# Kernel tuning notes

Hardware: AMD Instinct MI355X
Metric: run time of the kernel (lower is better)

The kernel has to match this reference:

```python
import jax, jax.numpy as jnp
from jax import lax
import numpy as np

DIM = 768
NUM_HEADS = 12
HEAD_DIM = DIM // NUM_HEADS
POOL = 8
LAM1_INIT = 0.5
LAM2_INIT = 0.5
EPS = 1e-6


def rmsnorm(x, w):
    # x / (||x||_2 / sqrt(d) + eps) * w
    d = x.shape[-1]
    rms = jnp.sqrt(jnp.sum(x * x, axis=-1, keepdims=True)) / jnp.sqrt(jnp.asarray(d, x.dtype))
    return x / (rms + EPS) * w


def setup_inputs() -> dict:
    key = jax.random.key(0)
    ks = jax.random.split(key, 10)
    B, H, W = 32, 32, 32
    N = H * W
    x = jax.random.normal(ks[0], (B, N, DIM), dtype=jnp.float32)
    Wqkv = jax.random.normal(ks[1], (3 * DIM, DIM), dtype=jnp.float32) * 0.02
    Wproj = jax.random.normal(ks[2], (DIM, DIM), dtype=jnp.float32) * 0.02
    bproj = jnp.zeros((DIM,), dtype=jnp.float32)
    Wpos = jax.random.normal(ks[3], (HEAD_DIM, HEAD_DIM), dtype=jnp.float32) * 0.02
    Wneg = jax.random.normal(ks[4], (HEAD_DIM, HEAD_DIM), dtype=jnp.float32) * 0.02
    conv_w = jax.random.normal(ks[5], (HEAD_DIM, 1, 3, 3), dtype=jnp.float32) * 0.1  # depthwise OIHW
    lam1 = jnp.asarray(LAM1_INIT, dtype=jnp.float32)
    lam2 = jnp.asarray(LAM2_INIT, dtype=jnp.float32)
    norm1_w = jnp.ones((HEAD_DIM,), dtype=jnp.float32)
    norm2_w = jnp.ones((HEAD_DIM,), dtype=jnp.float32)
    return {"x": x, "Wqkv": Wqkv, "Wproj": Wproj, "bproj": bproj, "Wpos": Wpos,
            "Wneg": Wneg, "conv_w": conv_w, "lam1": lam1, "lam2": lam2,
            "norm1_w": norm1_w, "norm2_w": norm2_w, "H": H, "W": W}


def reference(x, Wqkv, Wproj, bproj, Wpos, Wneg, conv_w, lam1, lam2, norm1_w, norm2_w, H, W):
    B, N, C = x.shape
    h, hd, p = NUM_HEADS, HEAD_DIM, POOL
    scale = hd ** -0.5
    # qkv projection -> [3, B, h, N, hd]
    qkv = (x @ Wqkv.T).reshape(B, N, 3, h, hd).transpose(2, 0, 3, 1, 4)
    q, k, v = qkv[0], qkv[1], qkv[2]
    # depthwise conv + GELU on q in spatial form
    q2 = q.reshape(B, h, H, W, hd).transpose(0, 1, 4, 2, 3).reshape(B * h, hd, H, W)
    qe = lax.conv_general_dilated(q2, conv_w, window_strides=(1, 1), padding='SAME',
                                  feature_group_count=hd,
                                  dimension_numbers=('NCHW', 'OIHW', 'NCHW'))
    qe = jax.nn.gelu(qe, approximate=False)
    # adaptive avg pool to (p, p): exact since H % p == 0
    qp = qe.reshape(B * h, hd, p, H // p, p, W // p).mean(axis=(3, 5))
    t_base = qp.reshape(B, h, hd, p, p).transpose(0, 1, 3, 4, 2).reshape(B, h, p * p, hd)
    # dynamic e+/e- embeddings from global query
    gq = q.mean(axis=2)  # [B, h, hd]
    t_pos = t_base + (gq @ Wpos.T)[:, :, None, :]
    t_neg = t_base + (gq @ Wneg.T)[:, :, None, :]
    # stage 1: pooled contrast tokens attend to k/v
    attn_pos = jax.nn.softmax(jnp.einsum('bhmd,bhnd->bhmn', t_pos, k) * scale, axis=-1)
    v_hat_pos = attn_pos @ v  # [B, h, p*p, hd]
    attn_neg = jax.nn.softmax(jnp.einsum('bhmd,bhnd->bhmn', t_neg, k) * scale, axis=-1)
    v_hat_neg = attn_neg @ v
    v_contrast = rmsnorm(v_hat_pos - lam1 * v_hat_neg, norm1_w) * (1.0 - LAM1_INIT)
    # stage 2: q attends to contrast tokens
    attn1 = jax.nn.softmax(jnp.einsum('bhnd,bhmd->bhnm', q, t_pos) * scale, axis=-1)
    attn2 = jax.nn.softmax(jnp.einsum('bhnd,bhmd->bhnm', q, t_neg) * scale, axis=-1)
    out_patch = (attn1 - lam2 * attn2) @ v_contrast  # [B, h, N, hd]
    out_patch = rmsnorm(out_patch, norm2_w) * (1.0 - LAM2_INIT)
    out_patch = out_patch.transpose(0, 2, 1, 3).reshape(B, N, C)
    out = out_patch @ Wproj.T + bproj
    return out
```

## Files before the change

### kernel.cpp

```cpp
#include <hip/hip_runtime.h>
#include <hip/hip_bf16.h>


typedef __attribute__((ext_vector_type(8))) short short8;
typedef __attribute__((ext_vector_type(4))) short bf16x4;
typedef __attribute__((ext_vector_type(4))) float f32x4;

#define DEV static __device__ __forceinline__

DEV unsigned short f2bf(float f) {
  unsigned int b; __builtin_memcpy(&b, &f, 4);
  unsigned int r = (b + 0x7FFFu + ((b >> 16) & 1u)) >> 16;
  return (unsigned short)r;
}
DEV float bf2f(unsigned short u) {
  unsigned int b = ((unsigned int)u) << 16;
  float f; __builtin_memcpy(&f, &b, 4);
  return f;
}

DEV void gload16(const unsigned short* g, unsigned short* l) {
  __builtin_amdgcn_global_load_lds(
      (const __attribute__((address_space(1))) unsigned int*)g,
      (__attribute__((address_space(3))) unsigned int*)l, 16, 0, 0);
}

constexpr size_t SZ_QKV = (size_t)32 * 12 * 1024 * 64 * 2;
constexpr size_t OFF_Q   = 0;
constexpr size_t OFF_K   = OFF_Q + SZ_QKV;
constexpr size_t OFF_VT  = OFF_K + SZ_QKV;
constexpr size_t OFF_TPB = OFF_VT + SZ_QKV;
constexpr size_t OFF_TNB = OFF_TPB + 3145728;
constexpr size_t OFF_VCT = OFF_TNB + 3145728;
constexpr size_t OFF_OP  = OFF_VCT + 6291456;
constexpr size_t OFF_XB  = OFF_OP + SZ_QKV;
constexpr size_t OFF_WQ  = OFF_XB + SZ_QKV;
constexpr size_t OFF_WP  = OFF_WQ + 3538944;
constexpr size_t OFF_EP  = OFF_WP + 1179648;
constexpr size_t OFF_EN  = OFF_EP + 98304;

__global__ __launch_bounds__(256) void cast_kernel(const float* __restrict__ src,
                                                   unsigned short* __restrict__ dst, int n4) {
  int i = blockIdx.x * 256 + threadIdx.x;
  if (i >= n4) return;
  float4 v = reinterpret_cast<const float4*>(src)[i];
  ushort4 o;
  o.x = f2bf(v.x); o.y = f2bf(v.y); o.z = f2bf(v.z); o.w = f2bf(v.w);
  reinterpret_cast<ushort4*>(dst)[i] = o;
}

__global__ __launch_bounds__(256) void gemm_qkv_kernel(const unsigned short* __restrict__ A,
    const unsigned short* __restrict__ Bm, unsigned short* __restrict__ q,
    unsigned short* __restrict__ k, unsigned short* __restrict__ vt) {
  __shared__ unsigned short As[2 * 128 * 32];
  __shared__ unsigned short Bs[2 * 128 * 32];
  const int t = threadIdx.x;
  const int lane = t & 63;
  const int w = t >> 6;
  const int wm = w >> 1, wn = w & 1;
  const int row0 = blockIdx.y * 128;
  const int col0 = blockIdx.x * 128;
  f32x4 acc[4][4];
#pragma unroll
  for (int i = 0; i < 4; ++i)
#pragma unroll
    for (int j = 0; j < 4; ++j) acc[i][j] = (f32x4){0.f, 0.f, 0.f, 0.f};
  const int l = lane & 15, g = lane >> 4;
  const int srow = lane >> 2, scol = (lane & 3) << 3;
  for (int k0 = 0; k0 < 768; k0 += 64) {
    __syncthreads();
#pragma unroll
    for (int kc = 0; kc < 2; ++kc)
#pragma unroll
      for (int j = 0; j < 2; ++j) {
        const int qs = w * 2 + j;
        const int r = qs * 16 + srow;
        const int cg = k0 + kc * 32 + scol;
        gload16(A + (size_t)(row0 + r) * 768 + cg, As + kc * 4096 + qs * 512);
        gload16(Bm + (size_t)(col0 + r) * 768 + cg, Bs + kc * 4096 + qs * 512);
      }
    __syncthreads();
#pragma unroll
    for (int kc = 0; kc < 2; ++kc) {
      short8 af[4], bfv[4];
#pragma unroll
      for (int mt = 0; mt < 4; ++mt)
        af[mt] = *reinterpret_cast<const short8*>(As + kc * 4096 + (wm * 64 + mt * 16 + l) * 32 + g * 8);
#pragma unroll
      for (int nt = 0; nt < 4; ++nt)
        bfv[nt] = *reinterpret_cast<const short8*>(Bs + kc * 4096 + (wn * 64 + nt * 16 + l) * 32 + g * 8);
#pragma unroll
      for (int mt = 0; mt < 4; ++mt)
#pragma unroll
        for (int nt = 0; nt < 4; ++nt)
          acc[mt][nt] = __builtin_amdgcn_mfma_f32_16x16x32_bf16(af[mt], bfv[nt], acc[mt][nt], 0, 0, 0);
    }
  }
  const int s_ = col0 / 768;
  if (s_ == 2) {
#pragma unroll
    for (int nt = 0; nt < 4; ++nt) {
      const int colin = wn * 64 + nt * 16 + l;
      const int head = ((col0 % 768) + colin) >> 6;
      const int d = colin & 63;
#pragma unroll
      for (int mt = 0; mt < 4; ++mt) {
        const int row = row0 + wm * 64 + mt * 16 + (g << 2);
        const int b = row >> 10, n = row & 1023;
        ushort4 pk;
        pk.x = f2bf(acc[mt][nt][0]); pk.y = f2bf(acc[mt][nt][1]);
        pk.z = f2bf(acc[mt][nt][2]); pk.w = f2bf(acc[mt][nt][3]);
        *reinterpret_cast<ushort4*>(vt + ((((size_t)b * 12 + head) * 64 + d) << 10) + n) = pk;
      }
    }
  } else {
    unsigned short* dst = (s_ == 0) ? q : k;
#pragma unroll
    for (int nt = 0; nt < 4; ++nt) {
      const int colin = wn * 64 + nt * 16 + l;
      const int head = ((col0 % 768) + colin) >> 6;
      const int d = colin & 63;
#pragma unroll
      for (int mt = 0; mt < 4; ++mt) {
#pragma unroll
        for (int r = 0; r < 4; ++r) {
          const int row = row0 + wm * 64 + mt * 16 + (g << 2) + r;
          const int b = row >> 10, n = row & 1023;
          dst[(((size_t)b * 12 + head) * 1024 + n) * 64 + d] = f2bf(acc[mt][nt][r]);
        }
      }
    }
  }
}

__global__ __launch_bounds__(256) void gq_embed_kernel(const unsigned short* __restrict__ qg,
    const float* __restrict__ Wpos, const float* __restrict__ Wneg,
    float* __restrict__ ep, float* __restrict__ en) {
  const int bh = blockIdx.x;
  const unsigned short* qp = qg + (size_t)bh * 65536;
  __shared__ float red2[32][64];
  __shared__ float gq_s[64];
  const int t = threadIdx.x;
  const int c8 = (t & 7) << 3;
  const int part = t >> 3;
  float s[8] = {0.f, 0.f, 0.f, 0.f, 0.f, 0.f, 0.f, 0.f};
  for (int i = 0; i < 32; ++i) {
    const short8 v = *reinterpret_cast<const short8*>(qp + (size_t)(part * 32 + i) * 64 + c8);
#pragma unroll
    for (int j = 0; j < 8; ++j) s[j] += bf2f((unsigned short)v[j]);
  }
#pragma unroll
  for (int j = 0; j < 8; ++j) red2[part][c8 + j] = s[j];
  __syncthreads();
  if (t < 64) {
    float s2 = 0.f;
    for (int p = 0; p < 32; ++p) s2 += red2[p][t];
    gq_s[t] = s2 * (1.0f / 1024.0f);
  }
  __syncthreads();
  if (t < 128) {
    const int d2 = t & 63;
    const float* Wm = (t < 64) ? Wpos : Wneg;
    float e = 0.f;
    for (int dd = 0; dd < 64; ++dd) e += gq_s[dd] * Wm[d2 * 64 + dd];
    (t < 64 ? ep : en)[bh * 64 + d2] = e;
  }
}

__global__ __launch_bounds__(256) void conv_pool_kernel(const unsigned short* __restrict__ qg,
    const float* __restrict__ conv_w, const float* __restrict__ ep,
    const float* __restrict__ en, unsigned short* __restrict__ t_pos,
    unsigned short* __restrict__ t_neg) {
  const int bh = blockIdx.x;
  const int quad = blockIdx.y;
  const unsigned short* qp = qg + (size_t)bh * 65536;
  __shared__ float pool_s[16][64];
  const int t = threadIdx.x;
  const int dg = t & 7, sp = t >> 3;
  const int d0 = dg << 3;
  float cw[3][3][8];
#pragma unroll
  for (int ky = 0; ky < 3; ++ky)
#pragma unroll
    for (int kx = 0; kx < 3; ++kx)
#pragma unroll
      for (int j = 0; j < 8; ++j)
        cw[ky][kx][j] = conv_w[(d0 + j) * 9 + ky * 3 + kx];
#pragma unroll
  for (int pyl = 0; pyl < 2; ++pyl) {
    float win[8] = {0.f, 0.f, 0.f, 0.f, 0.f, 0.f, 0.f, 0.f};
#pragma unroll
    for (int iy = 0; iy < 4; ++iy) {
      const int y = quad * 8 + pyl * 4 + iy;
      float a[8] = {0.f, 0.f, 0.f, 0.f, 0.f, 0.f, 0.f, 0.f};
#pragma unroll
      for (int ky = 0; ky < 3; ++ky) {
        const int yy = y + ky - 1;
        if (yy < 0 || yy > 31) continue;
#pragma unroll
        for (int kx = 0; kx < 3; ++kx) {
          const int xx = sp + kx - 1;
          if (xx < 0 || xx > 31) continue;
          const short8 v = *reinterpret_cast<const short8*>(qp + (size_t)(yy * 32 + xx) * 64 + d0);
#pragma unroll
          for (int j = 0; j < 8; ++j) a[j] += bf2f((unsigned short)v[j]) * cw[ky][kx][j];
        }
      }
#pragma unroll
      for (int j = 0; j < 8; ++j)
        win[j] += 0.5f * a[j] * (1.0f + erff(a[j] * 0.70710678118654752440f));
    }
#pragma unroll
    for (int j = 0; j < 8; ++j) {
      win[j] += __shfl_xor(win[j], 8);
      win[j] += __shfl_xor(win[j], 16);
    }
    if ((sp & 3) == 0) {
      const int px = sp >> 2;
#pragma unroll
      for (int j = 0; j < 8; ++j) pool_s[pyl * 8 + px][d0 + j] = win[j];
    }
  }
  __syncthreads();
#pragma unroll
  for (int i = 0; i < 4; ++i) {
    const int idx = i * 256 + t;
    const int m = idx >> 6, dd = idx & 63;
    const int mg = quad * 16 + m;
    const float base = pool_s[m][dd] * (1.0f / 16.0f);
    t_pos[(size_t)bh * 4096 + mg * 64 + dd] = f2bf(base + ep[bh * 64 + dd]);
    t_neg[(size_t)bh * 4096 + mg * 64 + dd] = f2bf(base + en[bh * 64 + dd]);
  }
}

__global__ __launch_bounds__(256) void stage1_kernel(const unsigned short* __restrict__ kg,
    const unsigned short* __restrict__ vtg, const unsigned short* __restrict__ tpb,
    const unsigned short* __restrict__ tnb, const float* __restrict__ lam1p,
    const float* __restrict__ norm1_w, float* __restrict__ vct) {
  const int bh = blockIdx.x;
  __shared__ unsigned short tp[64 * 72], tn[64 * 72];
  __shared__ unsigned short Ks[64 * 72], Vts[64 * 72];
  const int t = threadIdx.x;
  const int lane = t & 63;
  const int w = t >> 6;
  const int l = lane & 15, g = lane >> 4;
  for (int L = t; L < 512; L += 256) {
    const int r = L >> 3, c = (L & 7) << 3;
    *reinterpret_cast<short8*>(tp + r * 72 + c) =
        *reinterpret_cast<const short8*>(tpb + (size_t)bh * 4096 + r * 64 + c);
    *reinterpret_cast<short8*>(tn + r * 72 + c) =
        *reinterpret_cast<const short8*>(tnb + (size_t)bh * 4096 + r * 64 + c);
  }
  __syncthreads();
  short8 tf[2][2];
#pragma unroll
  for (int h = 0; h < 2; ++h) {
    tf[0][h] = *reinterpret_cast<const short8*>(tp + (w * 16 + l) * 72 + h * 32 + g * 8);
    tf[1][h] = *reinterpret_cast<const short8*>(tn + (w * 16 + l) * 72 + h * 32 + g * 8);
  }
  float Mo[2] = {-1e30f, -1e30f}, Lo[2] = {0.f, 0.f};
  f32x4 acc[2][4];
#pragma unroll
  for (int pp = 0; pp < 2; ++pp)
#pragma unroll
    for (int dt = 0; dt < 4; ++dt) acc[pp][dt] = (f32x4){0.f, 0.f, 0.f, 0.f};
  const size_t kbase = (size_t)bh * 65536;

  for (int n0 = 0; n0 < 1024; n0 += 64) {
    __syncthreads();
    for (int L = t; L < 512; L += 256) {
      const int r = L >> 3, c = (L & 7) << 3;
      *reinterpret_cast<short8*>(Ks + r * 72 + c) =
          *reinterpret_cast<const short8*>(kg + kbase + (size_t)(n0 + r) * 64 + c);
      *reinterpret_cast<short8*>(Vts + r * 72 + c) =
          *reinterpret_cast<const short8*>(vtg + kbase + (size_t)r * 1024 + n0 + c);
    }
    __syncthreads();
    short8 kf[4][2];
#pragma unroll
    for (int tile = 0; tile < 4; ++tile)
#pragma unroll
      for (int h = 0; h < 2; ++h)
        kf[tile][h] = *reinterpret_cast<const short8*>(Ks + (tile * 16 + l) * 72 + h * 32 + g * 8);
    bf16x4 pf[2][4];
#pragma unroll
    for (int pp = 0; pp < 2; ++pp) {
      f32x4 s[4];
#pragma unroll
      for (int tile = 0; tile < 4; ++tile) {
        s[tile] = (f32x4){0.f, 0.f, 0.f, 0.f};
#pragma unroll
        for (int h = 0; h < 2; ++h)
          s[tile] = __builtin_amdgcn_mfma_f32_16x16x32_bf16(kf[tile][h], tf[pp][h], s[tile], 0, 0, 0);
      }
      float p[4][4];
      float tmax = -1e30f;
#pragma unroll
      for (int tile = 0; tile < 4; ++tile)
#pragma unroll
        for (int r = 0; r < 4; ++r) {
          const float v = s[tile][r] * 0.125f;
          p[tile][r] = v;
          tmax = fmaxf(tmax, v);
        }
      tmax = fmaxf(tmax, __shfl_xor(tmax, 16));
      tmax = fmaxf(tmax, __shfl_xor(tmax, 32));
      const float nm = fmaxf(Mo[pp], tmax);
      const float al = __expf(Mo[pp] - nm);
      Mo[pp] = nm;
      float ps = 0.f;
#pragma unroll
      for (int tile = 0; tile < 4; ++tile)
#pragma unroll
        for (int r = 0; r < 4; ++r) {
          const float e = __expf(p[tile][r] - nm);
          p[tile][r] = e;
          ps += e;
        }
      ps += __shfl_xor(ps, 16);
      ps += __shfl_xor(ps, 32);
      Lo[pp] = Lo[pp] * al + ps;
#pragma unroll
      for (int tile = 0; tile < 4; ++tile) {
        bf16x4 pk;
        pk[0] = (short)f2bf(p[tile][0]); pk[1] = (short)f2bf(p[tile][1]);
        pk[2] = (short)f2bf(p[tile][2]); pk[3] = (short)f2bf(p[tile][3]);
        pf[pp][tile] = pk;
      }
      float ar[4];
#pragma unroll
      for (int r = 0; r < 4; ++r) ar[r] = __shfl(al, 4 * g + r);
#pragma unroll
      for (int dt = 0; dt < 4; ++dt)
#pragma unroll
        for (int r = 0; r < 4; ++r) acc[pp][dt][r] *= ar[r];
    }
#pragma unroll
    for (int tile = 0; tile < 4; ++tile)
#pragma unroll
      for (int dt = 0; dt < 4; ++dt) {
        const bf16x4 vf = *reinterpret_cast<const bf16x4*>(Vts + (dt * 16 + l) * 72 + tile * 16 + g * 4);
        acc[0][dt] = __builtin_amdgcn_mfma_f32_16x16x16bf16_1k(pf[0][tile], vf, acc[0][dt], 0, 0, 0);
        acc[1][dt] = __builtin_amdgcn_mfma_f32_16x16x16bf16_1k(pf[1][tile], vf, acc[1][dt], 0, 0, 0);
      }
  }
  const float inv0 = 1.f / Lo[0], inv1 = 1.f / Lo[1];
  float i1r[4], i2r[4];
#pragma unroll
  for (int r = 0; r < 4; ++r) {
    i1r[r] = __shfl(inv0, 4 * g + r);
    i2r[r] = __shfl(inv1, 4 * g + r);
  }
  const float lam1 = lam1p[0];
  float od[4][4], ss[4] = {0.f, 0.f, 0.f, 0.f};
#pragma unroll
  for (int dt = 0; dt < 4; ++dt)
#pragma unroll
    for (int r = 0; r < 4; ++r) {
      const float v = acc[0][dt][r] * i1r[r] - lam1 * (acc[1][dt][r] * i2r[r]);
      od[dt][r] = v;
      ss[r] += v * v;
    }
#pragma unroll
  for (int r = 0; r < 4; ++r) {
    ss[r] += __shfl_xor(ss[r], 1);
    ss[r] += __shfl_xor(ss[r], 2);
    ss[r] += __shfl_xor(ss[r], 4);
    ss[r] += __shfl_xor(ss[r], 8);
  }
  float sc[4];
#pragma unroll
  for (int r = 0; r < 4; ++r) sc[r] = 0.5f / (sqrtf(ss[r]) * 0.125f + 1e-6f);
  const int mb = w * 16 + 4 * g;
#pragma unroll
  for (int dt = 0; dt < 4; ++dt) {
    const int dd = dt * 16 + l;
    const float nw = norm1_w[dd];
#pragma unroll
    for (int r = 0; r < 4; ++r)
      vct[(size_t)bh * 4096 + dd * 64 + mb + r] = od[dt][r] * sc[r] * nw;
  }
}

__global__ __launch_bounds__(256) void stage2_kernel(const unsigned short* __restrict__ qg,
    const unsigned short* __restrict__ tpb, const unsigned short* __restrict__ tnb,
    const float* __restrict__ vct, const float* __restrict__ lam2p,
    const float* __restrict__ norm2_w, unsigned short* __restrict__ opb) {
  const int bh = blockIdx.x;
  const int q0 = blockIdx.y * 64;
  __shared__ unsigned short tp[64 * 72], tn[64 * 72], Qs[64 * 72], Vc[64 * 72];
  const int t = threadIdx.x;
  const int lane = t & 63;
  const int w = t >> 6;
  const int l = lane & 15, g = lane >> 4;
  for (int L = t; L < 512; L += 256) {
    const int r = L >> 3, c = (L & 7) << 3;
    *reinterpret_cast<short8*>(tp + r * 72 + c) =
        *reinterpret_cast<const short8*>(tpb + (size_t)bh * 4096 + r * 64 + c);
    *reinterpret_cast<short8*>(tn + r * 72 + c) =
        *reinterpret_cast<const short8*>(tnb + (size_t)bh * 4096 + r * 64 + c);
    *reinterpret_cast<short8*>(Qs + r * 72 + c) =
        *reinterpret_cast<const short8*>(qg + (size_t)bh * 65536 + (size_t)(q0 + r) * 64 + c);
  }
  for (int L = t; L < 4096; L += 256) {
    const int dd = L >> 6, m = L & 63;
    Vc[dd * 72 + m] = f2bf(vct[(size_t)bh * 4096 + L]);
  }
  __syncthreads();
  short8 qf[2];
#pragma unroll
  for (int h = 0; h < 2; ++h)
    qf[h] = *reinterpret_cast<const short8*>(Qs + (w * 16 + l) * 72 + h * 32 + g * 8);
  bf16x4 vcf[4][4];
#pragma unroll
  for (int tile = 0; tile < 4; ++tile)
#pragma unroll
    for (int dt = 0; dt < 4; ++dt)
      vcf[tile][dt] = *reinterpret_cast<const bf16x4*>(Vc + (dt * 16 + l) * 72 + tile * 16 + g * 4);
  bf16x4 pf[2][4];
#pragma unroll
  for (int pp = 0; pp < 2; ++pp) {
    const unsigned short* tm = pp ? tn : tp;
    f32x4 s[4];
#pragma unroll
    for (int tile = 0; tile < 4; ++tile) {
      s[tile] = (f32x4){0.f, 0.f, 0.f, 0.f};
#pragma unroll
      for (int h = 0; h < 2; ++h) {
        const short8 tfb = *reinterpret_cast<const short8*>(tm + (tile * 16 + l) * 72 + h * 32 + g * 8);
        s[tile] = __builtin_amdgcn_mfma_f32_16x16x32_bf16(tfb, qf[h], s[tile], 0, 0, 0);
      }
    }
    float p[4][4];
    float lmax = -1e30f;
#pragma unroll
    for (int tile = 0; tile < 4; ++tile)
#pragma unroll
      for (int r = 0; r < 4; ++r) {
        const float v = s[tile][r] * 0.125f;
        p[tile][r] = v;
        lmax = fmaxf(lmax, v);
      }
    lmax = fmaxf(lmax, __shfl_xor(lmax, 16));
    lmax = fmaxf(lmax, __shfl_xor(lmax, 32));
    float ps = 0.f;
#pragma unroll
    for (int tile = 0; tile < 4; ++tile)
#pragma unroll
      for (int r = 0; r < 4; ++r) {
        const float e = __expf(p[tile][r] - lmax);
        p[tile][r] = e;
        ps += e;
      }
    ps += __shfl_xor(ps, 16);
    ps += __shfl_xor(ps, 32);
    const float inv = 1.f / ps;
#pragma unroll
    for (int tile = 0; tile < 4; ++tile) {
      bf16x4 pk;
      pk[0] = (short)f2bf(p[tile][0] * inv); pk[1] = (short)f2bf(p[tile][1] * inv);
      pk[2] = (short)f2bf(p[tile][2] * inv); pk[3] = (short)f2bf(p[tile][3] * inv);
      pf[pp][tile] = pk;
    }
  }
  f32x4 a1[4], a2[4];
#pragma unroll
  for (int dt = 0; dt < 4; ++dt) {
    a1[dt] = (f32x4){0.f, 0.f, 0.f, 0.f};
    a2[dt] = (f32x4){0.f, 0.f, 0.f, 0.f};
  }
#pragma unroll
  for (int tile = 0; tile < 4; ++tile)
#pragma unroll
    for (int dt = 0; dt < 4; ++dt) {
      a1[dt] = __builtin_amdgcn_mfma_f32_16x16x16bf16_1k(pf[0][tile], vcf[tile][dt], a1[dt], 0, 0, 0);
      a2[dt] = __builtin_amdgcn_mfma_f32_16x16x16bf16_1k(pf[1][tile], vcf[tile][dt], a2[dt], 0, 0, 0);
    }
  const float lam2 = lam2p[0];
  float od[4][4], ss[4] = {0.f, 0.f, 0.f, 0.f};
#pragma unroll
  for (int dt = 0; dt < 4; ++dt)
#pragma unroll
    for (int r = 0; r < 4; ++r) {
      const float v = a1[dt][r] - lam2 * a2[dt][r];
      od[dt][r] = v;
      ss[r] += v * v;
    }
#pragma unroll
  for (int r = 0; r < 4; ++r) {
    ss[r] += __shfl_xor(ss[r], 1);
    ss[r] += __shfl_xor(ss[r], 2);
    ss[r] += __shfl_xor(ss[r], 4);
    ss[r] += __shfl_xor(ss[r], 8);
  }
  float sc[4];
#pragma unroll
  for (int r = 0; r < 4; ++r) sc[r] = 0.5f / (sqrtf(ss[r]) * 0.125f + 1e-6f);
  const int b = bh / 12, head = bh % 12;
  const size_t ob = ((size_t)b * 1024 + q0 + w * 16 + 4 * g) * 768 + head * 64;
#pragma unroll
  for (int dt = 0; dt < 4; ++dt) {
    const float nw = norm2_w[dt * 16 + l];
#pragma unroll
    for (int r = 0; r < 4; ++r)
      opb[ob + (size_t)r * 768 + dt * 16 + l] = f2bf(od[dt][r] * sc[r] * nw);
  }
}

__global__ __launch_bounds__(256) void gemm_proj_kernel(const unsigned short* __restrict__ A,
    const unsigned short* __restrict__ Bm, const float* __restrict__ bias,
    float* __restrict__ out) {
  __shared__ unsigned short As[2 * 128 * 32];
  __shared__ unsigned short Bs[2 * 128 * 32];
  const int t = threadIdx.x;
  const int lane = t & 63;
  const int w = t >> 6;
  const int wm = w >> 1, wn = w & 1;
  const int row0 = blockIdx.y * 128;
  const int col0 = blockIdx.x * 128;
  f32x4 acc[4][4];
#pragma unroll
  for (int i = 0; i < 4; ++i)
#pragma unroll
    for (int j = 0; j < 4; ++j) acc[i][j] = (f32x4){0.f, 0.f, 0.f, 0.f};
  const int l = lane & 15, g = lane >> 4;
  const int srow = lane >> 2, scol = (lane & 3) << 3;
  for (int k0 = 0; k0 < 768; k0 += 64) {
    __syncthreads();
#pragma unroll
    for (int kc = 0; kc < 2; ++kc)
#pragma unroll
      for (int j = 0; j < 2; ++j) {
        const int qs = w * 2 + j;
        const int r = qs * 16 + srow;
        const int cg = k0 + kc * 32 + scol;
        gload16(A + (size_t)(row0 + r) * 768 + cg, As + kc * 4096 + qs * 512);
        gload16(Bm + (size_t)(col0 + r) * 768 + cg, Bs + kc * 4096 + qs * 512);
      }
    __syncthreads();
#pragma unroll
    for (int kc = 0; kc < 2; ++kc) {
      short8 af[4], bfv[4];
#pragma unroll
      for (int mt = 0; mt < 4; ++mt)
        af[mt] = *reinterpret_cast<const short8*>(As + kc * 4096 + (wm * 64 + mt * 16 + l) * 32 + g * 8);
#pragma unroll
      for (int nt = 0; nt < 4; ++nt)
        bfv[nt] = *reinterpret_cast<const short8*>(Bs + kc * 4096 + (wn * 64 + nt * 16 + l) * 32 + g * 8);
#pragma unroll
      for (int mt = 0; mt < 4; ++mt)
#pragma unroll
        for (int nt = 0; nt < 4; ++nt)
          acc[mt][nt] = __builtin_amdgcn_mfma_f32_16x16x32_bf16(af[mt], bfv[nt], acc[mt][nt], 0, 0, 0);
    }
  }
#pragma unroll
  for (int nt = 0; nt < 4; ++nt) {
    const int col = col0 + wn * 64 + nt * 16 + l;
    const float bv = bias[col];
#pragma unroll
    for (int mt = 0; mt < 4; ++mt)
#pragma unroll
      for (int r = 0; r < 4; ++r) {
        const int row = row0 + wm * 64 + mt * 16 + (g << 2) + r;
        out[(size_t)row * 768 + col] = acc[mt][nt][r] + bv;
      }
  }
}

extern "C" void kernel_launch(void* const* d_in, const int* in_sizes, int n_in,
                              void* d_out, int out_size, void* d_ws, size_t ws_size,
                              hipStream_t stream) {
  (void)in_sizes; (void)n_in; (void)out_size; (void)ws_size;
  const float* x       = (const float*)d_in[0];
  const float* Wqkv    = (const float*)d_in[1];
  const float* Wproj   = (const float*)d_in[2];
  const float* bproj   = (const float*)d_in[3];
  const float* Wpos    = (const float*)d_in[4];
  const float* Wneg    = (const float*)d_in[5];
  const float* conv_w  = (const float*)d_in[6];
  const float* lam1    = (const float*)d_in[7];
  const float* lam2    = (const float*)d_in[8];
  const float* norm1_w = (const float*)d_in[9];
  const float* norm2_w = (const float*)d_in[10];
  float* out = (float*)d_out;
  char* ws = (char*)d_ws;
  unsigned short* qb   = (unsigned short*)(ws + OFF_Q);
  unsigned short* kb   = (unsigned short*)(ws + OFF_K);
  unsigned short* vtb  = (unsigned short*)(ws + OFF_VT);
  unsigned short* tpbb = (unsigned short*)(ws + OFF_TPB);
  unsigned short* tnbb = (unsigned short*)(ws + OFF_TNB);
  float* vctb          = (float*)(ws + OFF_VCT);
  unsigned short* opb  = (unsigned short*)(ws + OFF_OP);
  unsigned short* xb   = (unsigned short*)(ws + OFF_XB);
  unsigned short* wqb  = (unsigned short*)(ws + OFF_WQ);
  unsigned short* wpb  = (unsigned short*)(ws + OFF_WP);
  float* epb           = (float*)(ws + OFF_EP);
  float* enb           = (float*)(ws + OFF_EN);

  cast_kernel<<<dim3(6291456 / 256), dim3(256), 0, stream>>>(x, xb, 6291456);
  cast_kernel<<<dim3(442368 / 256), dim3(256), 0, stream>>>(Wqkv, wqb, 442368);
  cast_kernel<<<dim3(147456 / 256), dim3(256), 0, stream>>>(Wproj, wpb, 147456);
  gemm_qkv_kernel<<<dim3(18, 256), dim3(256), 0, stream>>>(xb, wqb, qb, kb, vtb);
  gq_embed_kernel<<<dim3(384), dim3(256), 0, stream>>>(qb, Wpos, Wneg, epb, enb);
  conv_pool_kernel<<<dim3(384, 4), dim3(256), 0, stream>>>(qb, conv_w, epb, enb, tpbb, tnbb);
  stage1_kernel<<<dim3(384), dim3(256), 0, stream>>>(kb, vtb, tpbb, tnbb, lam1, norm1_w, vctb);
  stage2_kernel<<<dim3(384, 16), dim3(256), 0, stream>>>(qb, tpbb, tnbb, vctb, lam2, norm2_w, opb);
  gemm_proj_kernel<<<dim3(6, 256), dim3(256), 0, stream>>>(opb, wpb, bproj, out);
}
```

Baseline: 453.9 us.

## Double-buffer GEMM LDS tiles, swizzle block order, split stage1 over N halves

Both GEMMs now double-buffer their LDS tiles, so the global-to-LDS load of the next K tile is issued before the MFMAs on the current tile, and they drop one barrier per iteration. Block indices are remapped with an XCD-style swizzle to improve L2 locality across the chiplets. stage1 now runs 512 threads per block, with two halves each processing half of the sequence, then merges the online-softmax partial results through shared memory. This costs more LDS per block and adds a merge step in exchange for more latency hiding and more parallelism in stage1, which only has 384 blocks.

```diff
diff --git a/kernel.cpp b/kernel.cpp
--- a/kernel.cpp
+++ b/kernel.cpp
@@ -49,17 +49,35 @@
   reinterpret_cast<ushort4*>(dst)[i] = o;
 }
 
+DEV void stage_tile(const unsigned short* __restrict__ A,
+                    const unsigned short* __restrict__ Bm,
+                    unsigned short* As, unsigned short* Bs,
+                    int row0, int col0, int k0, int w, int srow, int scol) {
+#pragma unroll
+  for (int kc = 0; kc < 2; ++kc)
+#pragma unroll
+    for (int j = 0; j < 2; ++j) {
+      const int qs = w * 2 + j;
+      const int r = qs * 16 + srow;
+      const int cg = k0 + kc * 32 + scol;
+      gload16(A + (size_t)(row0 + r) * 768 + cg, As + kc * 4096 + qs * 512);
+      gload16(Bm + (size_t)(col0 + r) * 768 + cg, Bs + kc * 4096 + qs * 512);
+    }
+}
+
 __global__ __launch_bounds__(256) void gemm_qkv_kernel(const unsigned short* __restrict__ A,
     const unsigned short* __restrict__ Bm, unsigned short* __restrict__ q,
     unsigned short* __restrict__ k, unsigned short* __restrict__ vt) {
-  __shared__ unsigned short As[2 * 128 * 32];
-  __shared__ unsigned short Bs[2 * 128 * 32];
+  __shared__ unsigned short As[2][8192];
+  __shared__ unsigned short Bs[2][8192];
   const int t = threadIdx.x;
   const int lane = t & 63;
   const int w = t >> 6;
   const int wm = w >> 1, wn = w & 1;
-  const int row0 = blockIdx.y * 128;
-  const int col0 = blockIdx.x * 128;
+  const int id = blockIdx.x;
+  const int swz = (id & 7) * 576 + (id >> 3);
+  const int row0 = (swz / 18) * 128;
+  const int col0 = (swz % 18) * 128;
   f32x4 acc[4][4];
 #pragma unroll
   for (int i = 0; i < 4; ++i)
@@ -67,34 +85,29 @@
     for (int j = 0; j < 4; ++j) acc[i][j] = (f32x4){0.f, 0.f, 0.f, 0.f};
   const int l = lane & 15, g = lane >> 4;
   const int srow = lane >> 2, scol = (lane & 3) << 3;
-  for (int k0 = 0; k0 < 768; k0 += 64) {
-    __syncthreads();
-#pragma unroll
-    for (int kc = 0; kc < 2; ++kc)
-#pragma unroll
-      for (int j = 0; j < 2; ++j) {
-        const int qs = w * 2 + j;
-        const int r = qs * 16 + srow;
-        const int cg = k0 + kc * 32 + scol;
-        gload16(A + (size_t)(row0 + r) * 768 + cg, As + kc * 4096 + qs * 512);
-        gload16(Bm + (size_t)(col0 + r) * 768 + cg, Bs + kc * 4096 + qs * 512);
-      }
-    __syncthreads();
+
+  stage_tile(A, Bm, As[0], Bs[0], row0, col0, 0, w, srow, scol);
+  __syncthreads();
+  for (int kt = 0; kt < 12; ++kt) {
+    const int cur = kt & 1;
+    if (kt < 11)
+      stage_tile(A, Bm, As[cur ^ 1], Bs[cur ^ 1], row0, col0, (kt + 1) * 64, w, srow, scol);
 #pragma unroll
     for (int kc = 0; kc < 2; ++kc) {
       short8 af[4], bfv[4];
 #pragma unroll
       for (int mt = 0; mt < 4; ++mt)
-        af[mt] = *reinterpret_cast<const short8*>(As + kc * 4096 + (wm * 64 + mt * 16 + l) * 32 + g * 8);
+        af[mt] = *reinterpret_cast<const short8*>(As[cur] + kc * 4096 + (wm * 64 + mt * 16 + l) * 32 + g * 8);
 #pragma unroll
       for (int nt = 0; nt < 4; ++nt)
-        bfv[nt] = *reinterpret_cast<const short8*>(Bs + kc * 4096 + (wn * 64 + nt * 16 + l) * 32 + g * 8);
+        bfv[nt] = *reinterpret_cast<const short8*>(Bs[cur] + kc * 4096 + (wn * 64 + nt * 16 + l) * 32 + g * 8);
 #pragma unroll
       for (int mt = 0; mt < 4; ++mt)
 #pragma unroll
         for (int nt = 0; nt < 4; ++nt)
           acc[mt][nt] = __builtin_amdgcn_mfma_f32_16x16x32_bf16(af[mt], bfv[nt], acc[mt][nt], 0, 0, 0);
     }
+    __syncthreads();
   }
   const int s_ = col0 / 768;
   if (s_ == 2) {
@@ -233,19 +246,24 @@
   }
 }
 
-__global__ __launch_bounds__(256) void stage1_kernel(const unsigned short* __restrict__ kg,
+__global__ __launch_bounds__(512) void stage1_kernel(const unsigned short* __restrict__ kg,
     const unsigned short* __restrict__ vtg, const unsigned short* __restrict__ tpb,
     const unsigned short* __restrict__ tnb, const float* __restrict__ lam1p,
     const float* __restrict__ norm1_w, float* __restrict__ vct) {
   const int bh = blockIdx.x;
-  __shared__ unsigned short tp[64 * 72], tn[64 * 72];
-  __shared__ unsigned short Ks[64 * 72], Vts[64 * 72];
+  __shared__ __align__(16) char smem[55296];
+  unsigned short* tp = (unsigned short*)(smem);
+  unsigned short* tn = (unsigned short*)(smem + 9216);
   const int t = threadIdx.x;
   const int lane = t & 63;
   const int w = t >> 6;
+  const int half = w >> 2, strip = w & 3;
+  const int th = t & 255;
   const int l = lane & 15, g = lane >> 4;
-  for (int L = t; L < 512; L += 256) {
-    const int r = L >> 3, c = (L & 7) << 3;
+  unsigned short* Ks  = (unsigned short*)(smem + 18432 + half * 18432);
+  unsigned short* Vts = (unsigned short*)(smem + 18432 + half * 18432 + 9216);
+  {
+    const int r = t >> 3, c = (t & 7) << 3;
     *reinterpret_cast<short8*>(tp + r * 72 + c) =
         *reinterpret_cast<const short8*>(tpb + (size_t)bh * 4096 + r * 64 + c);
     *reinterpret_cast<short8*>(tn + r * 72 + c) =
@@ -255,8 +273,8 @@
   short8 tf[2][2];
 #pragma unroll
   for (int h = 0; h < 2; ++h) {
-    tf[0][h] = *reinterpret_cast<const short8*>(tp + (w * 16 + l) * 72 + h * 32 + g * 8);
-    tf[1][h] = *reinterpret_cast<const short8*>(tn + (w * 16 + l) * 72 + h * 32 + g * 8);
+    tf[0][h] = *reinterpret_cast<const short8*>(tp + (strip * 16 + l) * 72 + h * 32 + g * 8);
+    tf[1][h] = *reinterpret_cast<const short8*>(tn + (strip * 16 + l) * 72 + h * 32 + g * 8);
   }
   float Mo[2] = {-1e30f, -1e30f}, Lo[2] = {0.f, 0.f};
   f32x4 acc[2][4];
@@ -266,9 +284,10 @@
     for (int dt = 0; dt < 4; ++dt) acc[pp][dt] = (f32x4){0.f, 0.f, 0.f, 0.f};
   const size_t kbase = (size_t)bh * 65536;
 
-  for (int n0 = 0; n0 < 1024; n0 += 64) {
+  for (int it = 0; it < 8; ++it) {
+    const int n0 = half * 512 + it * 64;
     __syncthreads();
-    for (int L = t; L < 512; L += 256) {
+    for (int L = th; L < 512; L += 256) {
       const int r = L >> 3, c = (L & 7) << 3;
       *reinterpret_cast<short8*>(Ks + r * 72 + c) =
           *reinterpret_cast<const short8*>(kg + kbase + (size_t)(n0 + r) * 64 + c);
@@ -344,41 +363,82 @@
         acc[1][dt] = __builtin_amdgcn_mfma_f32_16x16x16bf16_1k(pf[1][tile], vf, acc[1][dt], 0, 0, 0);
       }
   }
-  const float inv0 = 1.f / Lo[0], inv1 = 1.f / Lo[1];
-  float i1r[4], i2r[4];
-#pragma unroll
-  for (int r = 0; r < 4; ++r) {
-    i1r[r] = __shfl(inv0, 4 * g + r);
-    i2r[r] = __shfl(inv1, 4 * g + r);
-  }
-  const float lam1 = lam1p[0];
-  float od[4][4], ss[4] = {0.f, 0.f, 0.f, 0.f};
-#pragma unroll
-  for (int dt = 0; dt < 4; ++dt)
+  __syncthreads();
+  float* accS = (float*)(smem + 18432);
+  float* moS  = (float*)(smem + 51200);
+  float* loS  = (float*)(smem + 51712);
+  if (half == 1) {
+#pragma unroll
+    for (int pp = 0; pp < 2; ++pp) {
+#pragma unroll
+      for (int dt = 0; dt < 4; ++dt)
+        *reinterpret_cast<f32x4*>(accS + ((((strip * 2 + pp) * 4 + dt) * 64) + lane) * 4) = acc[pp][dt];
+      if (g == 0) {
+        moS[(strip * 2 + pp) * 16 + l] = Mo[pp];
+        loS[(strip * 2 + pp) * 16 + l] = Lo[pp];
+      }
+    }
+  }
+  __syncthreads();
+  if (half == 0) {
+#pragma unroll
+    for (int pp = 0; pp < 2; ++pp) {
+      const float m1v = moS[(strip * 2 + pp) * 16 + l];
+      const float l1v = loS[(strip * 2 + pp) * 16 + l];
+      const float nm = fmaxf(Mo[pp], m1v);
+      const float a0 = __expf(Mo[pp] - nm);
+      const float a1 = __expf(m1v - nm);
+      Lo[pp] = Lo[pp] * a0 + l1v * a1;
+      float a0r[4], a1r[4];
+#pragma unroll
+      for (int r = 0; r < 4; ++r) {
+        a0r[r] = __shfl(a0, 4 * g + r);
+        a1r[r] = __shfl(a1, 4 * g + r);
+      }
+#pragma unroll
+      for (int dt = 0; dt < 4; ++dt) {
+        const f32x4 o = *reinterpret_cast<const f32x4*>(accS + ((((strip * 2 + pp) * 4 + dt) * 64) + lane) * 4);
+#pragma unroll
+        for (int r = 0; r < 4; ++r)
+          acc[pp][dt][r] = acc[pp][dt][r] * a0r[r] + o[r] * a1r[r];
+      }
+    }
+    const float inv0 = 1.f / Lo[0], inv1 = 1.f / Lo[1];
+    float i1r[4], i2r[4];
 #pragma unroll
     for (int r = 0; r < 4; ++r) {
-      const float v = acc[0][dt][r] * i1r[r] - lam1 * (acc[1][dt][r] * i2r[r]);
-      od[dt][r] = v;
-      ss[r] += v * v;
-    }
-#pragma unroll
-  for (int r = 0; r < 4; ++r) {
-    ss[r] += __shfl_xor(ss[r], 1);
-    ss[r] += __shfl_xor(ss[r], 2);
-    ss[r] += __shfl_xor(ss[r], 4);
-    ss[r] += __shfl_xor(ss[r], 8);
-  }
-  float sc[4];
-#pragma unroll
-  for (int r = 0; r < 4; ++r) sc[r] = 0.5f / (sqrtf(ss[r]) * 0.125f + 1e-6f);
-  const int mb = w * 16 + 4 * g;
-#pragma unroll
-  for (int dt = 0; dt < 4; ++dt) {
-    const int dd = dt * 16 + l;
-    const float nw = norm1_w[dd];
-#pragma unroll
-    for (int r = 0; r < 4; ++r)
-      vct[(size_t)bh * 4096 + dd * 64 + mb + r] = od[dt][r] * sc[r] * nw;
+      i1r[r] = __shfl(inv0, 4 * g + r);
+      i2r[r] = __shfl(inv1, 4 * g + r);
+    }
+    const float lam1 = lam1p[0];
+    float od[4][4], ss[4] = {0.f, 0.f, 0.f, 0.f};
+#pragma unroll
+    for (int dt = 0; dt < 4; ++dt)
+#pragma unroll
+      for (int r = 0; r < 4; ++r) {
+        const float v = acc[0][dt][r] * i1r[r] - lam1 * (acc[1][dt][r] * i2r[r]);
+        od[dt][r] = v;
+        ss[r] += v * v;
+      }
+#pragma unroll
+    for (int r = 0; r < 4; ++r) {
+      ss[r] += __shfl_xor(ss[r], 1);
+      ss[r] += __shfl_xor(ss[r], 2);
+      ss[r] += __shfl_xor(ss[r], 4);
+      ss[r] += __shfl_xor(ss[r], 8);
+    }
+    float sc[4];
+#pragma unroll
+    for (int r = 0; r < 4; ++r) sc[r] = 0.5f / (sqrtf(ss[r]) * 0.125f + 1e-6f);
+    const int mb = strip * 16 + 4 * g;
+#pragma unroll
+    for (int dt = 0; dt < 4; ++dt) {
+      const int dd = dt * 16 + l;
+      const float nw = norm1_w[dd];
+#pragma unroll
+      for (int r = 0; r < 4; ++r)
+        vct[(size_t)bh * 4096 + dd * 64 + mb + r] = od[dt][r] * sc[r] * nw;
+    }
   }
 }
 
@@ -510,14 +570,16 @@
 __global__ __launch_bounds__(256) void gemm_proj_kernel(const unsigned short* __restrict__ A,
     const unsigned short* __restrict__ Bm, const float* __restrict__ bias,
     float* __restrict__ out) {
-  __shared__ unsigned short As[2 * 128 * 32];
-  __shared__ unsigned short Bs[2 * 128 * 32];
+  __shared__ unsigned short As[2][8192];
+  __shared__ unsigned short Bs[2][8192];
   const int t = threadIdx.x;
   const int lane = t & 63;
   const int w = t >> 6;
   const int wm = w >> 1, wn = w & 1;
-  const int row0 = blockIdx.y * 128;
-  const int col0 = blockIdx.x * 128;
+  const int id = blockIdx.x;
+  const int swz = (id & 7) * 192 + (id >> 3);
+  const int row0 = (swz / 6) * 128;
+  const int col0 = (swz % 6) * 128;
   f32x4 acc[4][4];
 #pragma unroll
   for (int i = 0; i < 4; ++i)
@@ -525,34 +587,29 @@
     for (int j = 0; j < 4; ++j) acc[i][j] = (f32x4){0.f, 0.f, 0.f, 0.f};
   const int l = lane & 15, g = lane >> 4;
   const int srow = lane >> 2, scol = (lane & 3) << 3;
-  for (int k0 = 0; k0 < 768; k0 += 64) {
-    __syncthreads();
-#pragma unroll
-    for (int kc = 0; kc < 2; ++kc)
-#pragma unroll
-      for (int j = 0; j < 2; ++j) {
-        const int qs = w * 2 + j;
-        const int r = qs * 16 + srow;
-        const int cg = k0 + kc * 32 + scol;
-        gload16(A + (size_t)(row0 + r) * 768 + cg, As + kc * 4096 + qs * 512);
-        gload16(Bm + (size_t)(col0 + r) * 768 + cg, Bs + kc * 4096 + qs * 512);
-      }
-    __syncthreads();
+
+  stage_tile(A, Bm, As[0], Bs[0], row0, col0, 0, w, srow, scol);
+  __syncthreads();
+  for (int kt = 0; kt < 12; ++kt) {
+    const int cur = kt & 1;
+    if (kt < 11)
+      stage_tile(A, Bm, As[cur ^ 1], Bs[cur ^ 1], row0, col0, (kt + 1) * 64, w, srow, scol);
 #pragma unroll
     for (int kc = 0; kc < 2; ++kc) {
       short8 af[4], bfv[4];
 #pragma unroll
       for (int mt = 0; mt < 4; ++mt)
-        af[mt] = *reinterpret_cast<const short8*>(As + kc * 4096 + (wm * 64 + mt * 16 + l) * 32 + g * 8);
+        af[mt] = *reinterpret_cast<const short8*>(As[cur] + kc * 4096 + (wm * 64 + mt * 16 + l) * 32 + g * 8);
 #pragma unroll
       for (int nt = 0; nt < 4; ++nt)
-        bfv[nt] = *reinterpret_cast<const short8*>(Bs + kc * 4096 + (wn * 64 + nt * 16 + l) * 32 + g * 8);
+        bfv[nt] = *reinterpret_cast<const short8*>(Bs[cur] + kc * 4096 + (wn * 64 + nt * 16 + l) * 32 + g * 8);
 #pragma unroll
       for (int mt = 0; mt < 4; ++mt)
 #pragma unroll
         for (int nt = 0; nt < 4; ++nt)
           acc[mt][nt] = __builtin_amdgcn_mfma_f32_16x16x32_bf16(af[mt], bfv[nt], acc[mt][nt], 0, 0, 0);
     }
+    __syncthreads();
   }
 #pragma unroll
   for (int nt = 0; nt < 4; ++nt) {
@@ -601,10 +658,10 @@
   cast_kernel<<<dim3(6291456 / 256), dim3(256), 0, stream>>>(x, xb, 6291456);
   cast_kernel<<<dim3(442368 / 256), dim3(256), 0, stream>>>(Wqkv, wqb, 442368);
   cast_kernel<<<dim3(147456 / 256), dim3(256), 0, stream>>>(Wproj, wpb, 147456);
-  gemm_qkv_kernel<<<dim3(18, 256), dim3(256), 0, stream>>>(xb, wqb, qb, kb, vtb);
+  gemm_qkv_kernel<<<dim3(4608), dim3(256), 0, stream>>>(xb, wqb, qb, kb, vtb);
   gq_embed_kernel<<<dim3(384), dim3(256), 0, stream>>>(qb, Wpos, Wneg, epb, enb);
   conv_pool_kernel<<<dim3(384, 4), dim3(256), 0, stream>>>(qb, conv_w, epb, enb, tpbb, tnbb);
-  stage1_kernel<<<dim3(384), dim3(256), 0, stream>>>(kb, vtb, tpbb, tnbb, lam1, norm1_w, vctb);
+  stage1_kernel<<<dim3(384), dim3(512), 0, stream>>>(kb, vtb, tpbb, tnbb, lam1, norm1_w, vctb);
   stage2_kernel<<<dim3(384, 16), dim3(256), 0, stream>>>(qb, tpbb, tnbb, vctb, lam2, norm2_w, opb);
-  gemm_proj_kernel<<<dim3(6, 256), dim3(256), 0, stream>>>(opb, wpb, bproj, out);
-}
+  gemm_proj_kernel<<<dim3(1536), dim3(256), 0, stream>>>(opb, wpb, bproj, out);
+}
```

Measured after the change: 474.9 us. +4.6%, slower.
